# Kernel tuning notes

Measured on AMD Instinct MI355X. Metric: run time of the kernel, lower is better.

The kernel has to match this reference:

```python
import jax, jax.numpy as jnp
import numpy as np

EPS = 1e-5  # torch InstanceNorm2d default eps

def instance_norm(x):
    # per-sample, per-channel normalization over spatial dims (affine=False)
    m = jnp.mean(x, axis=(2, 3), keepdims=True)
    v = jnp.var(x, axis=(2, 3), keepdims=True)
    return (x - m) * jax.lax.rsqrt(v + EPS)

def conv2d(x, w, b, stride, pad):
    y = jax.lax.conv_general_dilated(
        x, w, (stride, stride), [(pad, pad), (pad, pad)],
        dimension_numbers=('NCHW', 'OIHW', 'NCHW'))
    return y + b[None, :, None, None]

def res_block(x, w1, b1, w2, b2):
    out = conv2d(jax.nn.relu(instance_norm(x)), w1, b1, 1, 1)
    out = conv2d(jax.nn.relu(instance_norm(out)), w2, b2, 1, 1)
    return out + x

def res_block_strided(x, w1, b1, w2, b2, ws, bs):
    out = conv2d(jax.nn.relu(instance_norm(x)), w1, b1, 2, 1)
    out = conv2d(jax.nn.relu(instance_norm(out)), w2, b2, 1, 1)
    return out + conv2d(x, ws, bs, 2, 0)  # 1x1 strided skip projection

def setup_inputs() -> dict:
    key = jax.random.key(0)
    ks = jax.random.split(key, 12)
    B, N, C, H, W = 64, 1, 3, 256, 256
    TEXT, EMB, F, HEADS = 256, 512, 32, 5
    FH, FW = H // 16, W // 16  # 16, 16
    def rn(k, shape, scale=0.05):
        return jax.random.normal(k, shape, dtype=jnp.float32) * scale
    z = lambda *s: jnp.zeros(s, jnp.float32)
    return {
        'x': jax.random.normal(ks[0], (B, N, C, H, W), jnp.float32),
        'text_vector': jax.random.normal(ks[1], (B, TEXT), jnp.float32),
        'conv1_w': rn(ks[2], (F, C, 7, 7)),
        'conv1_b': z(F),
        'rbs_w1': rn(ks[3], (3, F, F, 3, 3)),  # 3 strided resblocks
        'rbs_b1': z(3, F),
        'rbs_w2': rn(ks[4], (3, F, F, 3, 3)),
        'rbs_b2': z(3, F),
        'rbs_ws': rn(ks[5], (3, F, F, 1, 1)),
        'rbs_bs': z(3, F),
        'rb_w1': rn(ks[6], (2, F, F, 3, 3)),  # 2 plain resblocks
        'rb_b1': z(2, F),
        'rb_w2': rn(ks[7], (2, F, F, 3, 3)),
        'rb_b2': z(2, F),
        'attn_w': rn(ks[8], (HEADS, FH * FW, TEXT)),  # torch Linear [out,in] per head
        'attn_b': z(HEADS, FH * FW),
        'final_w': rn(ks[9], (EMB, FH * FW * HEADS)),
        'final_b': z(EMB),
    }

def reference(x, text_vector, conv1_w, conv1_b, rbs_w1, rbs_b1, rbs_w2, rbs_b2,
              rbs_ws, rbs_bs, rb_w1, rb_b1, rb_w2, rb_b2, attn_w, attn_b,
              final_w, final_b):
    B, N, C, H, W = x.shape
    feat = x.reshape(B, N * C, H, W)
    feat = instance_norm(feat)
    feat = conv2d(feat, conv1_w, conv1_b, 2, 3)
    # block1 = strided + plain; block2 = strided + plain; block3 = strided
    feat = res_block_strided(feat, rbs_w1[0], rbs_b1[0], rbs_w2[0], rbs_b2[0], rbs_ws[0], rbs_bs[0])
    feat = res_block(feat, rb_w1[0], rb_b1[0], rb_w2[0], rb_b2[0])
    feat = res_block_strided(feat, rbs_w1[1], rbs_b1[1], rbs_w2[1], rbs_b2[1], rbs_ws[1], rbs_bs[1])
    feat = res_block(feat, rb_w1[1], rb_b1[1], rb_w2[1], rb_b2[1])
    feat = res_block_strided(feat, rbs_w1[2], rbs_b1[2], rbs_w2[2], rbs_b2[2], rbs_ws[2], rbs_bs[2])
    # feat: [B, 32, FH, FW]
    HEADS = attn_w.shape[0]
    FH, FW = feat.shape[2], feat.shape[3]
    # sigmoid-gated spatial attention logits per head: [B, HEADS, FH, FW]
    a = jax.nn.sigmoid(jnp.einsum('bt,hot->bho', text_vector, attn_w) + attn_b[None])
    a = a.reshape(B, HEADS, FH, FW)
    # channel scores: spatial sum of gate * feature -> [B, HEADS, C]
    scores = jnp.einsum('bhij,bcij->bhc', a, feat)
    probs = jax.nn.softmax(scores, axis=-1)  # old F.softmax over channel dim
    # weighted channel sum -> per-head attention map [B, HEADS, FH, FW]
    amaps = jnp.einsum('bhc,bcij->bhij', probs, feat)
    out = amaps.reshape(B, -1) @ final_w.T + final_b
    return out
```

## Files before the change

### kernel.cpp

```cpp
#include <hip/hip_runtime.h>
#include <cstdint>
#include <cstddef>

#define INORM_EPS 1e-5f

typedef _Float16 f16;
typedef f16 f16x8 __attribute__((ext_vector_type(8)));
typedef f16 f16x4 __attribute__((ext_vector_type(4)));
typedef float f32x4 __attribute__((ext_vector_type(4)));

__global__ __launch_bounds__(256) void prep(
    const float* __restrict__ rbs_w1, const float* __restrict__ rbs_w2,
    const float* __restrict__ rb_w1, const float* __restrict__ rb_w2,
    const float* __restrict__ rbs_ws, const float* __restrict__ conv1_w,
    float2* __restrict__ SP, f16* __restrict__ wp3, f16* __restrict__ wp1,
    f16* __restrict__ wp7) {
  int i = blockIdx.x * 256 + threadIdx.x;
  if (i < 20672) { SP[i] = make_float2(0.f, 0.f); return; }
  i -= 20672;
  if (i < 92160) {
    int mat = i / 9216, r = i % 9216;
    int p = r >> 10, f = (r >> 9) & 1, l = (r >> 3) & 63, j = r & 7;
    int co = f * 16 + (l & 15), ci = (l >> 4) * 8 + j;
    const float* src; int m;
    if (mat < 3) { src = rbs_w1; m = mat; }
    else if (mat < 6) { src = rbs_w2; m = mat - 3; }
    else if (mat < 8) { src = rb_w1; m = mat - 6; }
    else { src = rb_w2; m = mat - 8; }
    wp3[i] = (f16)src[m * 9216 + co * 288 + ci * 9 + p];
    return;
  }
  i -= 92160;
  if (i < 3072) {
    int mat = i / 1024, r = i % 1024;
    int f = r >> 9, l = (r >> 3) & 63, j = r & 7;
    wp1[i] = (f16)rbs_ws[mat * 1024 + (f * 16 + (l & 15)) * 32 + (l >> 4) * 8 + j];
    return;
  }
  i -= 3072;
  if (i >= 7168) return;
  int ky = i >> 10, f = (i >> 9) & 1, l = (i >> 3) & 63, j = i & 7;
  int k = (l >> 4) * 8 + j, kx = k >> 2, ci = k & 3;
  float v = 0.f;
  if (kx < 7 && ci < 3) v = conv1_w[(f * 16 + (l & 15)) * 147 + ci * 49 + ky * 7 + kx];
  wp7[i] = (f16)v;
}

__global__ __launch_bounds__(256) void stats_raw(const float* __restrict__ in,
                                                 float2* __restrict__ st, int HW) {
  const int map = blockIdx.x >> 3, chunk = blockIdx.x & 7;
  const int n4 = HW >> 5;
  const float4* p = (const float4*)(in + (size_t)map * HW + (size_t)chunk * (HW >> 3));
  float s = 0.f, ss = 0.f;
  for (int i = threadIdx.x; i < n4; i += 256) {
    float4 v = p[i];
    s += v.x + v.y + v.z + v.w;
    ss += v.x * v.x + v.y * v.y + v.z * v.z + v.w * v.w;
  }
  __shared__ float r0[256], r1[256];
  r0[threadIdx.x] = s;
  r1[threadIdx.x] = ss;
  __syncthreads();
  for (int off = 128; off > 0; off >>= 1) {
    if ((int)threadIdx.x < off) {
      r0[threadIdx.x] += r0[threadIdx.x + off];
      r1[threadIdx.x] += r1[threadIdx.x + off];
    }
    __syncthreads();
  }
  if (threadIdx.x == 0) {
    atomicAdd(&st[map].x, r0[0]);
    atomicAdd(&st[map].y, r1[0]);
  }
}

template <int W, int SKIP, int RPB>
__global__ __launch_bounds__(256) void conv3r(
    const f16* __restrict__ Rin, const float2* __restrict__ SPin, float inv_hw,
    const f16* __restrict__ wp, const float* __restrict__ bias,
    const float* __restrict__ bias2, const f16* __restrict__ skip,
    const f16* __restrict__ wps, f16* __restrict__ Rout,
    float2* __restrict__ ostats) {
  constexpr int TPR = W / 16;
  constexpr int LEN = (RPB * TPR) / 4;
  const int t = threadIdx.x, w = t >> 6, l = t & 63;
  const int n = l & 15, q = l >> 4;
  const int b = blockIdx.z;
  const int tx = w % TPR;
  const int y0 = blockIdx.x * RPB + (w / TPR) * LEN;
  const int x = (tx << 4) + n;
  const f16* Rb = Rin + (size_t)b * W * W * 32;

  f16x8 sc, sh;
#pragma unroll
  for (int j = 0; j < 8; j++) {
    float2 s = SPin[b * 32 + q * 8 + j];
    float mean = s.x * inv_hw;
    float rstd = rsqrtf(s.y * inv_hw - mean * mean + INORM_EPS);
    sc[j] = (f16)rstd;
    sh[j] = (f16)(-mean * rstd);
  }

  f16x8 wf[18];
#pragma unroll
  for (int i = 0; i < 18; i++) wf[i] = *(const f16x8*)(wp + i * 512 + l * 8);
  f16x8 wsf0, wsf1;
  if (SKIP == 2) {
    wsf0 = *(const f16x8*)(wps + l * 8);
    wsf1 = *(const f16x8*)(wps + 512 + l * 8);
  }
  float b0 = bias[n], b1 = bias[16 + n];
  if (SKIP == 2) { b0 += bias2[n]; b1 += bias2[16 + n]; }

  f16* ro = Rout + (size_t)b * W * W * 32;
  const f16* sb = skip ? skip + (size_t)b * (SKIP == 2 ? 4 : 1) * W * W * 32 : nullptr;

  bool okc[3];
#pragma unroll
  for (int kx = 0; kx < 3; kx++) okc[kx] = (unsigned)(x + kx - 1) < (unsigned)W;

  auto rowload = [&](int gy, f16x8* dst) {
    int gyc = min(max(gy, 0), W - 1);
#pragma unroll
    for (int kx = 0; kx < 3; kx++) {
      int gxc = min(max(x + kx - 1, 0), W - 1);
      dst[kx] = *(const f16x8*)(Rb + ((size_t)gyc * W + gxc) * 32 + q * 8);
    }
  };
  auto rownorm = [&](int gy, const f16x8* src, f16x8* dst) {
    bool okr = (unsigned)gy < (unsigned)W;
#pragma unroll
    for (int kx = 0; kx < 3; kx++) {
      f16x8 v = src[kx] * sc + sh;
#pragma unroll
      for (int e = 0; e < 8; e++) v[e] = v[e] > (f16)0 ? v[e] : (f16)0;
      f16x8 z = {};
      dst[kx] = (okr && okc[kx]) ? v : z;
    }
  };

  float sm0 = 0.f, sq0 = 0.f, sm1 = 0.f, sq1 = 0.f;
  f16x8 win[9];
  f16x8 pf[2][3];
#pragma unroll
  for (int jj = 0; jj < 3; jj++) rowload(y0 + jj - 1, &win[jj * 3]);
  if (LEN > 1) rowload(y0 + 2, pf[0]);
#pragma unroll
  for (int jj = 0; jj < 3; jj++) rownorm(y0 + jj - 1, &win[jj * 3], &win[jj * 3]);

#pragma unroll
  for (int i = 0; i < LEN; i++) {
    int y = y0 + i;
    if (i + 2 < LEN) rowload(y0 + i + 3, pf[(i + 1) & 1]);
    f32x4 acc0 = {0.f, 0.f, 0.f, 0.f}, acc1 = {0.f, 0.f, 0.f, 0.f};
#pragma unroll
    for (int ky = 0; ky < 3; ky++) {
      int slot = (i + ky) % 3;
#pragma unroll
      for (int kx = 0; kx < 3; kx++) {
        f16x8 a = win[slot * 3 + kx];
        acc0 = __builtin_amdgcn_mfma_f32_16x16x32_f16(a, wf[2 * (ky * 3 + kx)], acc0, 0, 0, 0);
        acc1 = __builtin_amdgcn_mfma_f32_16x16x32_f16(a, wf[2 * (ky * 3 + kx) + 1], acc1, 0, 0, 0);
      }
    }
    if (SKIP == 2) {
      const int Ws = 2 * W;
      f16x8 as = *(const f16x8*)(sb + ((size_t)(2 * y) * Ws + 2 * x) * 32 + q * 8);
      acc0 = __builtin_amdgcn_mfma_f32_16x16x32_f16(as, wsf0, acc0, 0, 0, 0);
      acc1 = __builtin_amdgcn_mfma_f32_16x16x32_f16(as, wsf1, acc1, 0, 0, 0);
    }
#pragma unroll
    for (int r = 0; r < 4; r++) {
      size_t px = (size_t)y * W + (tx << 4) + q * 4 + r;
      float v0 = acc0[r] + b0;
      float v1 = acc1[r] + b1;
      if (SKIP == 1) {
        v0 += (float)sb[px * 32 + n];
        v1 += (float)sb[px * 32 + 16 + n];
      }
      ro[px * 32 + n] = (f16)v0;
      ro[px * 32 + 16 + n] = (f16)v1;
      sm0 += v0; sq0 += v0 * v0;
      sm1 += v1; sq1 += v1 * v1;
    }
    if (i + 1 < LEN) rownorm(y0 + i + 2, pf[i & 1], &win[(i % 3) * 3]);
  }
  if (ostats) {
    sm0 += __shfl_xor(sm0, 16); sm0 += __shfl_xor(sm0, 32);
    sq0 += __shfl_xor(sq0, 16); sq0 += __shfl_xor(sq0, 32);
    sm1 += __shfl_xor(sm1, 16); sm1 += __shfl_xor(sm1, 32);
    sq1 += __shfl_xor(sq1, 16); sq1 += __shfl_xor(sq1, 32);
    if (l < 16) {
      atomicAdd(&ostats[b * 32 + n].x, sm0);
      atomicAdd(&ostats[b * 32 + n].y, sq0);
      atomicAdd(&ostats[b * 32 + 16 + n].x, sm1);
      atomicAdd(&ostats[b * 32 + 16 + n].y, sq1);
    }
  }
}

template <int WIN, int STRIDE, int SKIP, int RPB>
__global__ __launch_bounds__(256) void conv3n(
    const f16* __restrict__ Rin, const float2* __restrict__ SPin, float inv_hw,
    const f16* __restrict__ wp, const float* __restrict__ bias,
    const float* __restrict__ bias2, const f16* __restrict__ skip,
    const f16* __restrict__ wps, f16* __restrict__ Rout,
    float2* __restrict__ ostats) {
  constexpr int WOUT = WIN / STRIDE;
  constexpr int TPR = WOUT / 16;
  constexpr int UNITS = TPR * RPB;
  constexpr int U = UNITS / 4;
  static_assert(U >= 1, "need at least one unit per wave");
  constexpr int NB = (U >= 3) ? 3 : ((U >= 2) ? 2 : 1);
  const int t = threadIdx.x, w = t >> 6, l = t & 63;
  const int n = l & 15, q = l >> 4;
  const int b = blockIdx.z;
  const int yb = blockIdx.x * RPB;
  const f16* Rb = Rin + (size_t)b * WIN * WIN * 32;

  f16x8 sc, sh;
#pragma unroll
  for (int j = 0; j < 8; j++) {
    float2 s = SPin[b * 32 + q * 8 + j];
    float mean = s.x * inv_hw;
    float rstd = rsqrtf(s.y * inv_hw - mean * mean + INORM_EPS);
    sc[j] = (f16)rstd;
    sh[j] = (f16)(-mean * rstd);
  }

  f16x8 wf[18];
#pragma unroll
  for (int i = 0; i < 18; i++) wf[i] = *(const f16x8*)(wp + i * 512 + l * 8);
  f16x8 wsf0, wsf1;
  if (SKIP == 2) {
    wsf0 = *(const f16x8*)(wps + l * 8);
    wsf1 = *(const f16x8*)(wps + 512 + l * 8);
  }
  float b0 = bias[n], b1 = bias[16 + n];
  if (SKIP == 2) { b0 += bias2[n]; b1 += bias2[16 + n]; }

  f16* ro = Rout + (size_t)b * WOUT * WOUT * 32;
  const f16* sb = skip ? skip + (size_t)b * (SKIP == 2 ? 4 : 1) * WOUT * WOUT * 32 : nullptr;

  auto load_u = [&](int u, f16x8* a) {
    int ty = u / TPR, tx = u % TPR;
    int y = yb + ty;
#pragma unroll
    for (int kx = 0; kx < 3; kx++) {
      int gx = STRIDE * ((tx << 4) + n) + kx - 1;
      int gxc = min(max(gx, 0), WIN - 1);
#pragma unroll
      for (int ky = 0; ky < 3; ky++) {
        int gy = STRIDE * y + ky - 1;
        int gyc = min(max(gy, 0), WIN - 1);
        a[ky * 3 + kx] = *(const f16x8*)(Rb + ((size_t)gyc * WIN + gxc) * 32 + q * 8);
      }
    }
  };
  auto norm_u = [&](int u, f16x8* a) {
    int ty = u / TPR, tx = u % TPR;
    int y = yb + ty;
#pragma unroll
    for (int kx = 0; kx < 3; kx++) {
      int gx = STRIDE * ((tx << 4) + n) + kx - 1;
      bool okx = (unsigned)gx < (unsigned)WIN;
#pragma unroll
      for (int ky = 0; ky < 3; ky++) {
        int gy = STRIDE * y + ky - 1;
        bool ok = okx && ((unsigned)gy < (unsigned)WIN);
        f16x8 v = a[ky * 3 + kx] * sc + sh;
#pragma unroll
        for (int e = 0; e < 8; e++) v[e] = v[e] > (f16)0 ? v[e] : (f16)0;
        f16x8 z = {};
        a[ky * 3 + kx] = ok ? v : z;
      }
    }
  };

  float sm0 = 0.f, sq0 = 0.f, sm1 = 0.f, sq1 = 0.f;
  f16x8 buf[NB][9];
  load_u(w, buf[0]);
  if (U > 1) load_u(w + 4, buf[1 % NB]);
#pragma unroll
  for (int i = 0; i < U; i++) {
    int u = w + 4 * i;
    if (i + 2 < U) load_u(u + 8, buf[(i + 2) % NB]);
    f16x8* a = buf[i % NB];
    norm_u(u, a);
    int ty = u / TPR, tx = u % TPR;
    int y = yb + ty, x0 = tx << 4;
    f32x4 acc0 = {0.f, 0.f, 0.f, 0.f}, acc1 = {0.f, 0.f, 0.f, 0.f};
#pragma unroll
    for (int p = 0; p < 9; p++) {
      acc0 = __builtin_amdgcn_mfma_f32_16x16x32_f16(a[p], wf[2 * p], acc0, 0, 0, 0);
      acc1 = __builtin_amdgcn_mfma_f32_16x16x32_f16(a[p], wf[2 * p + 1], acc1, 0, 0, 0);
    }
    if (SKIP == 2) {
      const int Ws = 2 * WOUT;
      f16x8 as = *(const f16x8*)(sb + ((size_t)(2 * y) * Ws + 2 * (x0 + n)) * 32 + q * 8);
      acc0 = __builtin_amdgcn_mfma_f32_16x16x32_f16(as, wsf0, acc0, 0, 0, 0);
      acc1 = __builtin_amdgcn_mfma_f32_16x16x32_f16(as, wsf1, acc1, 0, 0, 0);
    }
#pragma unroll
    for (int r = 0; r < 4; r++) {
      size_t px = (size_t)y * WOUT + x0 + q * 4 + r;
      float v0 = acc0[r] + b0;
      float v1 = acc1[r] + b1;
      if (SKIP == 1) {
        v0 += (float)sb[px * 32 + n];
        v1 += (float)sb[px * 32 + 16 + n];
      }
      ro[px * 32 + n] = (f16)v0;
      ro[px * 32 + 16 + n] = (f16)v1;
      sm0 += v0; sq0 += v0 * v0;
      sm1 += v1; sq1 += v1 * v1;
    }
  }
  if (ostats) {
    sm0 += __shfl_xor(sm0, 16); sm0 += __shfl_xor(sm0, 32);
    sq0 += __shfl_xor(sq0, 16); sq0 += __shfl_xor(sq0, 32);
    sm1 += __shfl_xor(sm1, 16); sm1 += __shfl_xor(sm1, 32);
    sq1 += __shfl_xor(sq1, 16); sq1 += __shfl_xor(sq1, 32);
    if (l < 16) {
      atomicAdd(&ostats[b * 32 + n].x, sm0);
      atomicAdd(&ostats[b * 32 + n].y, sq0);
      atomicAdd(&ostats[b * 32 + 16 + n].x, sm1);
      atomicAdd(&ostats[b * 32 + 16 + n].y, sq1);
    }
  }
}

__global__ __launch_bounds__(256) void conv7(
    const float* __restrict__ x, const float2* __restrict__ SPx,
    const f16* __restrict__ wp, const float* __restrict__ bias,
    f16* __restrict__ Rout, float2* __restrict__ ostats) {
  __shared__ f16 lds[13 * 131 * 8];
  const int t = threadIdx.x, w = t >> 6, l = t & 63;
  const int n = l & 15, q = l >> 4;
  const int b = blockIdx.z;
  const int yb = blockIdx.x * 4;
  const float* Xb = x + (size_t)b * 3 * 65536;
  float mn[3], rs[3];
#pragma unroll
  for (int ci = 0; ci < 3; ci++) {
    float2 s = SPx[b * 3 + ci];
    mn[ci] = s.x * (1.f / 65536.f);
    rs[ci] = rsqrtf(s.y * (1.f / 65536.f) - mn[ci] * mn[ci] + INORM_EPS);
  }
  f16x8 wf[14];
#pragma unroll
  for (int i = 0; i < 14; i++) wf[i] = *(const f16x8*)(wp + i * 512 + l * 8);
  float b0 = bias[n], b1 = bias[16 + n];

  for (int idx = t; idx < 13 * 262; idx += 256) {
    int ri = idx / 262, cl = idx - ri * 262;
    int row = 2 * yb - 3 + ri, col = cl - 3;
    bool ok = ((unsigned)row < 256u) && ((unsigned)col < 256u);
    f16x4 v = {};
    if (ok) {
      const float* p = Xb + (size_t)row * 256 + col;
      v[0] = (f16)((p[0] - mn[0]) * rs[0]);
      v[1] = (f16)((p[65536] - mn[1]) * rs[1]);
      v[2] = (f16)((p[131072] - mn[2]) * rs[2]);
    }
    *(f16x4*)(lds + ((ri * 131 + (cl >> 1)) * 8) + (cl & 1) * 4) = v;
  }
  __syncthreads();

  float sm0 = 0.f, sq0 = 0.f, sm1 = 0.f, sq1 = 0.f;
  f16* ro = Rout + (size_t)b * 16384 * 32;

#pragma unroll
  for (int seg = 0; seg < 2; seg++) {
    const int tx = w + seg * 4;
    const int x0 = tx * 16;
    const int u = x0 + n + q;
#pragma unroll
    for (int i = 0; i < 4; i++) {
      int y = yb + i;
      f32x4 acc0 = {0.f, 0.f, 0.f, 0.f}, acc1 = {0.f, 0.f, 0.f, 0.f};
#pragma unroll
      for (int ky = 0; ky < 7; ky++) {
        f16x8 a = *(const f16x8*)(lds + ((2 * i + ky) * 131 + u) * 8);
        acc0 = __builtin_amdgcn_mfma_f32_16x16x32_f16(a, wf[2 * ky], acc0, 0, 0, 0);
        acc1 = __builtin_amdgcn_mfma_f32_16x16x32_f16(a, wf[2 * ky + 1], acc1, 0, 0, 0);
      }
#pragma unroll
      for (int r = 0; r < 4; r++) {
        size_t px = (size_t)y * 128 + x0 + q * 4 + r;
        float v0 = acc0[r] + b0;
        float v1 = acc1[r] + b1;
        ro[px * 32 + n] = (f16)v0;
        ro[px * 32 + 16 + n] = (f16)v1;
        sm0 += v0; sq0 += v0 * v0;
        sm1 += v1; sq1 += v1 * v1;
      }
    }
  }
  sm0 += __shfl_xor(sm0, 16); sm0 += __shfl_xor(sm0, 32);
  sq0 += __shfl_xor(sq0, 16); sq0 += __shfl_xor(sq0, 32);
  sm1 += __shfl_xor(sm1, 16); sm1 += __shfl_xor(sm1, 32);
  sq1 += __shfl_xor(sq1, 16); sq1 += __shfl_xor(sq1, 32);
  if (l < 16) {
    atomicAdd(&ostats[b * 32 + n].x, sm0);
    atomicAdd(&ostats[b * 32 + n].y, sq0);
    atomicAdd(&ostats[b * 32 + 16 + n].x, sm1);
    atomicAdd(&ostats[b * 32 + 16 + n].y, sq1);
  }
}

__global__ __launch_bounds__(256) void gates_kernel(
    const float* __restrict__ text, const float* __restrict__ attn_w,
    const float* __restrict__ attn_b, float* __restrict__ G) {
  __shared__ float s_text[64 * 257];
  __shared__ float s_w[16 * 256];
  const int t = threadIdx.x, wv = t >> 6, lane = t & 63;
  const int o0 = blockIdx.x * 16;
  for (int d = t; d < 16384; d += 256) {
    int b = d >> 8, k = d & 255;
    s_text[b * 257 + k] = text[d];
  }
  for (int d = t; d < 4096; d += 256) s_w[d] = attn_w[(size_t)o0 * 256 + d];
  __syncthreads();
  float acc[4];
#pragma unroll
  for (int j = 0; j < 4; j++) acc[j] = attn_b[o0 + wv * 4 + j];
  for (int k = 0; k < 256; k++) {
    float tv = s_text[lane * 257 + k];
#pragma unroll
    for (int j = 0; j < 4; j++) acc[j] = fmaf(s_w[(wv * 4 + j) * 256 + k], tv, acc[j]);
  }
#pragma unroll
  for (int j = 0; j < 4; j++) {
    int o = o0 + wv * 4 + j;
    G[o * 64 + lane] = 1.f / (1.f + __expf(-acc[j]));
  }
}

__global__ __launch_bounds__(256) void scores_kernel(
    const f16* __restrict__ feat, const float* __restrict__ G,
    float* __restrict__ amapT) {
  __shared__ float s_feat[256 * 33];
  __shared__ float s_gate[1280];
  __shared__ float s_scores[5 * 32];
  __shared__ float s_probs[5 * 32];
  const int b = blockIdx.x;
  const int t = threadIdx.x;

  for (int i = t; i < 8192; i += 256)
    s_feat[(i >> 5) * 33 + (i & 31)] = (float)feat[(size_t)b * 8192 + i];
  for (int i = t; i < 1280; i += 256) s_gate[i] = G[i * 64 + b];
  __syncthreads();

  if (t < 160) {
    int h = t >> 5, c = t & 31;
    float acc = 0.f;
    for (int ij = 0; ij < 256; ij++) acc += s_gate[h * 256 + ij] * s_feat[ij * 33 + c];
    s_scores[t] = acc;
  }
  __syncthreads();

  if (t < 5) {
    float mx = -1e30f;
    for (int c = 0; c < 32; c++) mx = fmaxf(mx, s_scores[t * 32 + c]);
    float sum = 0.f;
    for (int c = 0; c < 32; c++) {
      float e = __expf(s_scores[t * 32 + c] - mx);
      s_probs[t * 32 + c] = e;
      sum += e;
    }
    float inv = 1.f / sum;
    for (int c = 0; c < 32; c++) s_probs[t * 32 + c] *= inv;
  }
  __syncthreads();

  for (int h = 0; h < 5; h++) {
    float acc = 0.f;
    for (int c = 0; c < 32; c++) acc += s_probs[h * 32 + c] * s_feat[t * 33 + c];
    amapT[(h * 256 + t) * 64 + b] = acc;
  }
}

__global__ __launch_bounds__(256) void final_kernel(
    const float* __restrict__ amapT, const float* __restrict__ final_w,
    const float* __restrict__ final_b, float* __restrict__ out) {
  __shared__ float s_w[4 * 1280];
  __shared__ float s_red[4][4][64];
  const int t = threadIdx.x, wv = t >> 6, lane = t & 63;
  const int e0 = blockIdx.x * 4;
  for (int d = t; d < 5120; d += 256) s_w[d] = final_w[(size_t)e0 * 1280 + d];
  __syncthreads();
  const int k0 = wv * 320;
  float acc[4] = {0.f, 0.f, 0.f, 0.f};
  for (int k = k0; k < k0 + 320; k++) {
    float av = amapT[k * 64 + lane];
#pragma unroll
    for (int e = 0; e < 4; e++) acc[e] = fmaf(s_w[e * 1280 + k], av, acc[e]);
  }
#pragma unroll
  for (int e = 0; e < 4; e++) s_red[wv][e][lane] = acc[e];
  __syncthreads();
  if (wv == 0) {
#pragma unroll
    for (int e = 0; e < 4; e++) {
      float v = s_red[0][e][lane] + s_red[1][e][lane] + s_red[2][e][lane] +
                s_red[3][e][lane] + final_b[e0 + e];
      out[(size_t)lane * 512 + e0 + e] = v;
    }
  }
}

extern "C" void kernel_launch(void* const* d_in, const int* in_sizes, int n_in,
                              void* d_out, int out_size, void* d_ws, size_t ws_size,
                              hipStream_t stream) {
  (void)in_sizes; (void)n_in; (void)out_size; (void)ws_size;
  const float* x       = (const float*)d_in[0];
  const float* text    = (const float*)d_in[1];
  const float* conv1_w = (const float*)d_in[2];
  const float* conv1_b = (const float*)d_in[3];
  const float* rbs_w1  = (const float*)d_in[4];
  const float* rbs_b1  = (const float*)d_in[5];
  const float* rbs_w2  = (const float*)d_in[6];
  const float* rbs_b2  = (const float*)d_in[7];
  const float* rbs_ws  = (const float*)d_in[8];
  const float* rbs_bs  = (const float*)d_in[9];
  const float* rb_w1   = (const float*)d_in[10];
  const float* rb_b1   = (const float*)d_in[11];
  const float* rb_w2   = (const float*)d_in[12];
  const float* rb_b2   = (const float*)d_in[13];
  const float* attn_w  = (const float*)d_in[14];
  const float* attn_b  = (const float*)d_in[15];
  const float* final_w = (const float*)d_in[16];
  const float* final_b = (const float*)d_in[17];
  float* out = (float*)d_out;

  char* wsb = (char*)d_ws;
  f16*   R128 = (f16*)(wsb + 35145728);
  f16*   R64a = (f16*)(wsb + 102254592);
  f16*   R64b = (f16*)(wsb + 119031808);
  f16*   R64c = (f16*)(wsb + 135809024);
  f16*   R32a = (f16*)(wsb + 152586240);
  f16*   R32b = (f16*)(wsb + 156780544);
  f16*   R32c = (f16*)(wsb + 160974848);
  f16*   R16a = (f16*)(wsb + 165169152);
  f16*   R16b = (f16*)(wsb + 166217728);
  float2* SP  = (float2*)(wsb + 167266304);
  float2* SPx = (float2*)(wsb + 167430144);
  f16*   wp3  = (f16*)(wsb + 167431680);
  f16*   wp1  = (f16*)(wsb + 167616000);
  f16*   wp7  = (f16*)(wsb + 167622144);
  float* G     = (float*)(wsb + 167636480);
  float* amapT = (float*)(wsb + 167964160);
  float2* SP0 = SP + 0 * 2048;
  float2* SP1 = SP + 1 * 2048;
  float2* SP2 = SP + 2 * 2048;
  float2* SP3 = SP + 3 * 2048;
  float2* SP4 = SP + 4 * 2048;
  float2* SP5 = SP + 5 * 2048;
  float2* SP6 = SP + 6 * 2048;
  float2* SP7 = SP + 7 * 2048;
  float2* SP8 = SP + 8 * 2048;
  float2* SP9 = SP + 9 * 2048;

  prep<<<481, 256, 0, stream>>>(rbs_w1, rbs_w2, rb_w1, rb_w2, rbs_ws, conv1_w,
                                SP, wp3, wp1, wp7);
  stats_raw<<<1536, 256, 0, stream>>>(x, SPx, 65536);

  conv7<<<dim3(32, 1, 64), 256, 0, stream>>>(x, SPx, wp7, conv1_b, R128, SP0);

  conv3n<128, 2, 0, 4><<<dim3(16, 1, 64), 256, 0, stream>>>(
      R128, SP0, 1.f / 16384.f, wp3, rbs_b1, nullptr, nullptr, nullptr, R64a, SP1);
  conv3r<64, 2, 4><<<dim3(16, 1, 64), 256, 0, stream>>>(
      R64a, SP1, 1.f / 4096.f, wp3 + 3 * 9216, rbs_b2, rbs_bs, R128, wp1, R64b, SP2);

  conv3r<64, 0, 4><<<dim3(16, 1, 64), 256, 0, stream>>>(
      R64b, SP2, 1.f / 4096.f, wp3 + 6 * 9216, rb_b1, nullptr, nullptr, nullptr, R64c, SP3);
  conv3r<64, 1, 4><<<dim3(16, 1, 64), 256, 0, stream>>>(
      R64c, SP3, 1.f / 4096.f, wp3 + 8 * 9216, rb_b2, nullptr, R64b, nullptr, R64a, SP4);

  conv3n<64, 2, 0, 4><<<dim3(8, 1, 64), 256, 0, stream>>>(
      R64a, SP4, 1.f / 4096.f, wp3 + 1 * 9216, rbs_b1 + 32, nullptr, nullptr, nullptr, R32a, SP5);
  conv3r<32, 2, 2><<<dim3(16, 1, 64), 256, 0, stream>>>(
      R32a, SP5, 1.f / 1024.f, wp3 + 4 * 9216, rbs_b2 + 32, rbs_bs + 32, R64a, wp1 + 1024, R32b, SP6);

  conv3r<32, 0, 2><<<dim3(16, 1, 64), 256, 0, stream>>>(
      R32b, SP6, 1.f / 1024.f, wp3 + 7 * 9216, rb_b1 + 32, nullptr, nullptr, nullptr, R32c, SP7);
  conv3r<32, 1, 2><<<dim3(16, 1, 64), 256, 0, stream>>>(
      R32c, SP7, 1.f / 1024.f, wp3 + 9 * 9216, rb_b2 + 32, nullptr, R32b, nullptr, R32a, SP8);

  conv3n<32, 2, 0, 4><<<dim3(4, 1, 64), 256, 0, stream>>>(
      R32a, SP8, 1.f / 1024.f, wp3 + 2 * 9216, rbs_b1 + 64, nullptr, nullptr, nullptr, R16a, SP9);
  conv3n<16, 1, 2, 4><<<dim3(4, 1, 64), 256, 0, stream>>>(
      R16a, SP9, 1.f / 256.f, wp3 + 5 * 9216, rbs_b2 + 64, rbs_bs + 64, R32a, wp1 + 2048, R16b, nullptr);

  gates_kernel<<<80, 256, 0, stream>>>(text, attn_w, attn_b, G);
  scores_kernel<<<64, 256, 0, stream>>>(R16b, G, amapT);
  final_kernel<<<128, 256, 0, stream>>>(amapT, final_w, final_b, out);
}
```

Baseline: 362.5 us.

## Add LDS-staged stride-2 conv kernel and split conv7 across column halves

Adds a new conv3s2l kernel for the stride-2 3x3 convolutions. It stages the normalized and ReLU'd input tile in LDS with even and odd columns de-interleaved, so each MFMA operand is a contiguous LDS read, and it applies the normalize/ReLU once per element. This replaces conv3n for the first two strided blocks, using two x-halves for the 128 input. conv7 is also split across two column halves, which doubles the grid and shrinks the per-block LDS footprint to raise occupancy, at the cost of re-reading halo columns.

```diff
diff --git a/kernel.cpp b/kernel.cpp
--- a/kernel.cpp
+++ b/kernel.cpp
@@ -330,15 +330,110 @@
   }
 }
 
+template <int WIN>
+__global__ __launch_bounds__(256) void conv3s2l(
+    const f16* __restrict__ Rin, const float2* __restrict__ SPin, float inv_hw,
+    const f16* __restrict__ wp, const float* __restrict__ bias,
+    f16* __restrict__ Rout, float2* __restrict__ ostats) {
+  constexpr int WOUT = WIN / 2;
+  __shared__ f16 lds[4 * 9 * 66 * 8];
+  const int t = threadIdx.x, w = t >> 6, l = t & 63;
+  const int n = l & 15, q = l >> 4;
+  const int b = blockIdx.z;
+  const int yb = blockIdx.x * 4;
+  const int xh = blockIdx.y;
+  const f16* Rb = Rin + (size_t)b * WIN * WIN * 32;
+
+  const int qs = t & 3;
+  f16x8 scs, shs;
+#pragma unroll
+  for (int j = 0; j < 8; j++) {
+    float2 s = SPin[b * 32 + qs * 8 + j];
+    float mean = s.x * inv_hw;
+    float rstd = rsqrtf(s.y * inv_hw - mean * mean + INORM_EPS);
+    scs[j] = (f16)rstd;
+    shs[j] = (f16)(-mean * rstd);
+  }
+
+  for (int idx = t; idx < 2340; idx += 256) {
+    int ri = idx / 260, rem = idx - ri * 260;
+    int lc = rem >> 2;
+    int gr = 2 * yb - 1 + ri, gc = 64 * xh - 1 + lc;
+    bool ok = ((unsigned)gr < (unsigned)WIN) && ((unsigned)gc < (unsigned)WIN);
+    int grc = ok ? gr : 0, gcc = ok ? gc : 0;
+    f16x8 v = *(const f16x8*)(Rb + ((size_t)grc * WIN + gcc) * 32 + qs * 8);
+    v = v * scs + shs;
+#pragma unroll
+    for (int e = 0; e < 8; e++) v[e] = v[e] > (f16)0 ? v[e] : (f16)0;
+    f16x8 z = {};
+    if (!ok) v = z;
+    int sl = (lc & 1) ? (lc >> 1) : 32 + (lc >> 1);
+    *(f16x8*)(lds + qs * 4752 + (ri * 66 + sl) * 8) = v;
+  }
+
+  f16x8 wf[18];
+#pragma unroll
+  for (int i = 0; i < 18; i++) wf[i] = *(const f16x8*)(wp + i * 512 + l * 8);
+  float b0 = bias[n], b1 = bias[16 + n];
+  __syncthreads();
+
+  float sm0 = 0.f, sq0 = 0.f, sm1 = 0.f, sq1 = 0.f;
+  f16* ro = Rout + (size_t)b * WOUT * WOUT * 32;
+  const f16* lq = lds + q * 4752;
+
+#pragma unroll
+  for (int i = 0; i < 2; i++) {
+    int u = w + 4 * i;
+    int ty = u >> 1, tx = u & 1;
+    int m = tx * 16 + n;
+    f32x4 acc0 = {0.f, 0.f, 0.f, 0.f}, acc1 = {0.f, 0.f, 0.f, 0.f};
+#pragma unroll
+    for (int ky = 0; ky < 3; ky++) {
+      int ri = 2 * ty + ky;
+      f16x8 a0 = *(const f16x8*)(lq + (ri * 66 + 32 + m) * 8);
+      f16x8 a1 = *(const f16x8*)(lq + (ri * 66 + m) * 8);
+      f16x8 a2 = *(const f16x8*)(lq + (ri * 66 + 33 + m) * 8);
+      acc0 = __builtin_amdgcn_mfma_f32_16x16x32_f16(a0, wf[2 * (ky * 3 + 0)], acc0, 0, 0, 0);
+      acc1 = __builtin_amdgcn_mfma_f32_16x16x32_f16(a0, wf[2 * (ky * 3 + 0) + 1], acc1, 0, 0, 0);
+      acc0 = __builtin_amdgcn_mfma_f32_16x16x32_f16(a1, wf[2 * (ky * 3 + 1)], acc0, 0, 0, 0);
+      acc1 = __builtin_amdgcn_mfma_f32_16x16x32_f16(a1, wf[2 * (ky * 3 + 1) + 1], acc1, 0, 0, 0);
+      acc0 = __builtin_amdgcn_mfma_f32_16x16x32_f16(a2, wf[2 * (ky * 3 + 2)], acc0, 0, 0, 0);
+      acc1 = __builtin_amdgcn_mfma_f32_16x16x32_f16(a2, wf[2 * (ky * 3 + 2) + 1], acc1, 0, 0, 0);
+    }
+    int y = yb + ty, x0 = xh * 32 + tx * 16;
+#pragma unroll
+    for (int r = 0; r < 4; r++) {
+      size_t px = (size_t)y * WOUT + x0 + q * 4 + r;
+      float v0 = acc0[r] + b0;
+      float v1 = acc1[r] + b1;
+      ro[px * 32 + n] = (f16)v0;
+      ro[px * 32 + 16 + n] = (f16)v1;
+      sm0 += v0; sq0 += v0 * v0;
+      sm1 += v1; sq1 += v1 * v1;
+    }
+  }
+  sm0 += __shfl_xor(sm0, 16); sm0 += __shfl_xor(sm0, 32);
+  sq0 += __shfl_xor(sq0, 16); sq0 += __shfl_xor(sq0, 32);
+  sm1 += __shfl_xor(sm1, 16); sm1 += __shfl_xor(sm1, 32);
+  sq1 += __shfl_xor(sq1, 16); sq1 += __shfl_xor(sq1, 32);
+  if (l < 16) {
+    atomicAdd(&ostats[b * 32 + n].x, sm0);
+    atomicAdd(&ostats[b * 32 + n].y, sq0);
+    atomicAdd(&ostats[b * 32 + 16 + n].x, sm1);
+    atomicAdd(&ostats[b * 32 + 16 + n].y, sq1);
+  }
+}
+
 __global__ __launch_bounds__(256) void conv7(
     const float* __restrict__ x, const float2* __restrict__ SPx,
     const f16* __restrict__ wp, const float* __restrict__ bias,
     f16* __restrict__ Rout, float2* __restrict__ ostats) {
-  __shared__ f16 lds[13 * 131 * 8];
+  __shared__ f16 lds[13 * 67 * 8];
   const int t = threadIdx.x, w = t >> 6, l = t & 63;
   const int n = l & 15, q = l >> 4;
   const int b = blockIdx.z;
   const int yb = blockIdx.x * 4;
+  const int xh = blockIdx.y;
   const float* Xb = x + (size_t)b * 3 * 65536;
   float mn[3], rs[3];
 #pragma unroll
@@ -352,9 +447,9 @@
   for (int i = 0; i < 14; i++) wf[i] = *(const f16x8*)(wp + i * 512 + l * 8);
   float b0 = bias[n], b1 = bias[16 + n];
 
-  for (int idx = t; idx < 13 * 262; idx += 256) {
-    int ri = idx / 262, cl = idx - ri * 262;
-    int row = 2 * yb - 3 + ri, col = cl - 3;
+  for (int idx = t; idx < 13 * 134; idx += 256) {
+    int ri = idx / 134, cl = idx - ri * 134;
+    int row = 2 * yb - 3 + ri, col = 128 * xh - 3 + cl;
     bool ok = ((unsigned)row < 256u) && ((unsigned)col < 256u);
     f16x4 v = {};
     if (ok) {
@@ -363,38 +458,34 @@
       v[1] = (f16)((p[65536] - mn[1]) * rs[1]);
       v[2] = (f16)((p[131072] - mn[2]) * rs[2]);
     }
-    *(f16x4*)(lds + ((ri * 131 + (cl >> 1)) * 8) + (cl & 1) * 4) = v;
+    *(f16x4*)(lds + ((ri * 67 + (cl >> 1)) * 8) + (cl & 1) * 4) = v;
   }
   __syncthreads();
 
   float sm0 = 0.f, sq0 = 0.f, sm1 = 0.f, sq1 = 0.f;
   f16* ro = Rout + (size_t)b * 16384 * 32;
 
-#pragma unroll
-  for (int seg = 0; seg < 2; seg++) {
-    const int tx = w + seg * 4;
-    const int x0 = tx * 16;
-    const int u = x0 + n + q;
-#pragma unroll
-    for (int i = 0; i < 4; i++) {
-      int y = yb + i;
-      f32x4 acc0 = {0.f, 0.f, 0.f, 0.f}, acc1 = {0.f, 0.f, 0.f, 0.f};
-#pragma unroll
-      for (int ky = 0; ky < 7; ky++) {
-        f16x8 a = *(const f16x8*)(lds + ((2 * i + ky) * 131 + u) * 8);
-        acc0 = __builtin_amdgcn_mfma_f32_16x16x32_f16(a, wf[2 * ky], acc0, 0, 0, 0);
-        acc1 = __builtin_amdgcn_mfma_f32_16x16x32_f16(a, wf[2 * ky + 1], acc1, 0, 0, 0);
-      }
-#pragma unroll
-      for (int r = 0; r < 4; r++) {
-        size_t px = (size_t)y * 128 + x0 + q * 4 + r;
-        float v0 = acc0[r] + b0;
-        float v1 = acc1[r] + b1;
-        ro[px * 32 + n] = (f16)v0;
-        ro[px * 32 + 16 + n] = (f16)v1;
-        sm0 += v0; sq0 += v0 * v0;
-        sm1 += v1; sq1 += v1 * v1;
-      }
+  const int x0 = xh * 64 + w * 16;
+  const int u = w * 16 + n + q;
+#pragma unroll
+  for (int i = 0; i < 4; i++) {
+    int y = yb + i;
+    f32x4 acc0 = {0.f, 0.f, 0.f, 0.f}, acc1 = {0.f, 0.f, 0.f, 0.f};
+#pragma unroll
+    for (int ky = 0; ky < 7; ky++) {
+      f16x8 a = *(const f16x8*)(lds + ((2 * i + ky) * 67 + u) * 8);
+      acc0 = __builtin_amdgcn_mfma_f32_16x16x32_f16(a, wf[2 * ky], acc0, 0, 0, 0);
+      acc1 = __builtin_amdgcn_mfma_f32_16x16x32_f16(a, wf[2 * ky + 1], acc1, 0, 0, 0);
+    }
+#pragma unroll
+    for (int r = 0; r < 4; r++) {
+      size_t px = (size_t)y * 128 + x0 + q * 4 + r;
+      float v0 = acc0[r] + b0;
+      float v1 = acc1[r] + b1;
+      ro[px * 32 + n] = (f16)v0;
+      ro[px * 32 + 16 + n] = (f16)v1;
+      sm0 += v0; sq0 += v0 * v0;
+      sm1 += v1; sq1 += v1 * v1;
     }
   }
   sm0 += __shfl_xor(sm0, 16); sm0 += __shfl_xor(sm0, 32);
@@ -566,10 +657,10 @@
                                 SP, wp3, wp1, wp7);
   stats_raw<<<1536, 256, 0, stream>>>(x, SPx, 65536);
 
-  conv7<<<dim3(32, 1, 64), 256, 0, stream>>>(x, SPx, wp7, conv1_b, R128, SP0);
-
-  conv3n<128, 2, 0, 4><<<dim3(16, 1, 64), 256, 0, stream>>>(
-      R128, SP0, 1.f / 16384.f, wp3, rbs_b1, nullptr, nullptr, nullptr, R64a, SP1);
+  conv7<<<dim3(32, 2, 64), 256, 0, stream>>>(x, SPx, wp7, conv1_b, R128, SP0);
+
+  conv3s2l<128><<<dim3(16, 2, 64), 256, 0, stream>>>(
+      R128, SP0, 1.f / 16384.f, wp3, rbs_b1, R64a, SP1);
   conv3r<64, 2, 4><<<dim3(16, 1, 64), 256, 0, stream>>>(
       R64a, SP1, 1.f / 4096.f, wp3 + 3 * 9216, rbs_b2, rbs_bs, R128, wp1, R64b, SP2);
 
@@ -578,8 +669,8 @@
   conv3r<64, 1, 4><<<dim3(16, 1, 64), 256, 0, stream>>>(
       R64c, SP3, 1.f / 4096.f, wp3 + 8 * 9216, rb_b2, nullptr, R64b, nullptr, R64a, SP4);
 
-  conv3n<64, 2, 0, 4><<<dim3(8, 1, 64), 256, 0, stream>>>(
-      R64a, SP4, 1.f / 4096.f, wp3 + 1 * 9216, rbs_b1 + 32, nullptr, nullptr, nullptr, R32a, SP5);
+  conv3s2l<64><<<dim3(8, 1, 64), 256, 0, stream>>>(
+      R64a, SP4, 1.f / 4096.f, wp3 + 1 * 9216, rbs_b1 + 32, R32a, SP5);
   conv3r<32, 2, 2><<<dim3(16, 1, 64), 256, 0, stream>>>(
       R32a, SP5, 1.f / 1024.f, wp3 + 4 * 9216, rbs_b2 + 32, rbs_bs + 32, R64a, wp1 + 1024, R32b, SP6);
 
```

After: 391.2 us. +7.9%, slower.

## Merge input stats into prep kernel and double rows per conv block

Applied to the files above, without the earlier changes.

Folds the raw-input statistics reduction into the weight-prep kernel as extra blocks. Each block now writes a per-chunk partial sum instead of using atomics, and conv7 reduces the 8 partials itself, which removes a launch and the dependency on zeroed SPx. The conv3r/conv3n launches also double rows-per-block, halving grid size, to cut redundant halo and weight loads per block. The risks are lower occupancy and parallelism at small spatial sizes (e.g. only 2x64 blocks for the 16/32 stages) and a larger workspace region at offset 0.

```diff
diff --git a/kernel.cpp b/kernel.cpp
--- a/kernel.cpp
+++ b/kernel.cpp
@@ -9,15 +9,41 @@
 typedef f16 f16x4 __attribute__((ext_vector_type(4)));
 typedef float f32x4 __attribute__((ext_vector_type(4)));
 
-__global__ __launch_bounds__(256) void prep(
+__global__ __launch_bounds__(256) void prep_stats(
     const float* __restrict__ rbs_w1, const float* __restrict__ rbs_w2,
     const float* __restrict__ rb_w1, const float* __restrict__ rb_w2,
     const float* __restrict__ rbs_ws, const float* __restrict__ conv1_w,
-    float2* __restrict__ SP, f16* __restrict__ wp3, f16* __restrict__ wp1,
-    f16* __restrict__ wp7) {
-  int i = blockIdx.x * 256 + threadIdx.x;
-  if (i < 20672) { SP[i] = make_float2(0.f, 0.f); return; }
-  i -= 20672;
+    const float* __restrict__ x, float2* __restrict__ SP,
+    f16* __restrict__ wp3, f16* __restrict__ wp1, f16* __restrict__ wp7,
+    float2* __restrict__ SPx8) {
+  const int bx = blockIdx.x;
+  if (bx >= 480) {
+    const int g = bx - 480;
+    const int map = g >> 3, chunk = g & 7;
+    const float4* p = (const float4*)(x + (size_t)map * 65536 + (size_t)chunk * 8192);
+    float s = 0.f, ss = 0.f;
+    for (int i = threadIdx.x; i < 2048; i += 256) {
+      float4 v = p[i];
+      s += v.x + v.y + v.z + v.w;
+      ss += v.x * v.x + v.y * v.y + v.z * v.z + v.w * v.w;
+    }
+    __shared__ float r0[256], r1[256];
+    r0[threadIdx.x] = s;
+    r1[threadIdx.x] = ss;
+    __syncthreads();
+    for (int off = 128; off > 0; off >>= 1) {
+      if ((int)threadIdx.x < off) {
+        r0[threadIdx.x] += r0[threadIdx.x + off];
+        r1[threadIdx.x] += r1[threadIdx.x + off];
+      }
+      __syncthreads();
+    }
+    if (threadIdx.x == 0) SPx8[map * 8 + chunk] = make_float2(r0[0], r1[0]);
+    return;
+  }
+  int i = bx * 256 + threadIdx.x;
+  if (i < 20480) { SP[i] = make_float2(0.f, 0.f); return; }
+  i -= 20480;
   if (i < 92160) {
     int mat = i / 9216, r = i % 9216;
     int p = r >> 10, f = (r >> 9) & 1, l = (r >> 3) & 63, j = r & 7;
@@ -44,34 +70,6 @@
   float v = 0.f;
   if (kx < 7 && ci < 3) v = conv1_w[(f * 16 + (l & 15)) * 147 + ci * 49 + ky * 7 + kx];
   wp7[i] = (f16)v;
-}
-
-__global__ __launch_bounds__(256) void stats_raw(const float* __restrict__ in,
-                                                 float2* __restrict__ st, int HW) {
-  const int map = blockIdx.x >> 3, chunk = blockIdx.x & 7;
-  const int n4 = HW >> 5;
-  const float4* p = (const float4*)(in + (size_t)map * HW + (size_t)chunk * (HW >> 3));
-  float s = 0.f, ss = 0.f;
-  for (int i = threadIdx.x; i < n4; i += 256) {
-    float4 v = p[i];
-    s += v.x + v.y + v.z + v.w;
-    ss += v.x * v.x + v.y * v.y + v.z * v.z + v.w * v.w;
-  }
-  __shared__ float r0[256], r1[256];
-  r0[threadIdx.x] = s;
-  r1[threadIdx.x] = ss;
-  __syncthreads();
-  for (int off = 128; off > 0; off >>= 1) {
-    if ((int)threadIdx.x < off) {
-      r0[threadIdx.x] += r0[threadIdx.x + off];
-      r1[threadIdx.x] += r1[threadIdx.x + off];
-    }
-    __syncthreads();
-  }
-  if (threadIdx.x == 0) {
-    atomicAdd(&st[map].x, r0[0]);
-    atomicAdd(&st[map].y, r1[0]);
-  }
 }
 
 template <int W, int SKIP, int RPB>
@@ -331,7 +329,7 @@
 }
 
 __global__ __launch_bounds__(256) void conv7(
-    const float* __restrict__ x, const float2* __restrict__ SPx,
+    const float* __restrict__ x, const float2* __restrict__ SPx8,
     const f16* __restrict__ wp, const float* __restrict__ bias,
     f16* __restrict__ Rout, float2* __restrict__ ostats) {
   __shared__ f16 lds[13 * 131 * 8];
@@ -343,9 +341,14 @@
   float mn[3], rs[3];
 #pragma unroll
   for (int ci = 0; ci < 3; ci++) {
-    float2 s = SPx[b * 3 + ci];
-    mn[ci] = s.x * (1.f / 65536.f);
-    rs[ci] = rsqrtf(s.y * (1.f / 65536.f) - mn[ci] * mn[ci] + INORM_EPS);
+    float sx = 0.f, sxx = 0.f;
+#pragma unroll
+    for (int c = 0; c < 8; c++) {
+      float2 v = SPx8[(b * 3 + ci) * 8 + c];
+      sx += v.x; sxx += v.y;
+    }
+    mn[ci] = sx * (1.f / 65536.f);
+    rs[ci] = rsqrtf(sxx * (1.f / 65536.f) - mn[ci] * mn[ci] + INORM_EPS);
   }
   f16x8 wf[14];
 #pragma unroll
@@ -535,6 +538,7 @@
   float* out = (float*)d_out;
 
   char* wsb = (char*)d_ws;
+  float2* SPx8 = (float2*)(wsb + 0);
   f16*   R128 = (f16*)(wsb + 35145728);
   f16*   R64a = (f16*)(wsb + 102254592);
   f16*   R64b = (f16*)(wsb + 119031808);
@@ -545,7 +549,6 @@
   f16*   R16a = (f16*)(wsb + 165169152);
   f16*   R16b = (f16*)(wsb + 166217728);
   float2* SP  = (float2*)(wsb + 167266304);
-  float2* SPx = (float2*)(wsb + 167430144);
   f16*   wp3  = (f16*)(wsb + 167431680);
   f16*   wp1  = (f16*)(wsb + 167616000);
   f16*   wp7  = (f16*)(wsb + 167622144);
@@ -562,35 +565,34 @@
   float2* SP8 = SP + 8 * 2048;
   float2* SP9 = SP + 9 * 2048;
 
-  prep<<<481, 256, 0, stream>>>(rbs_w1, rbs_w2, rb_w1, rb_w2, rbs_ws, conv1_w,
-                                SP, wp3, wp1, wp7);
-  stats_raw<<<1536, 256, 0, stream>>>(x, SPx, 65536);
-
-  conv7<<<dim3(32, 1, 64), 256, 0, stream>>>(x, SPx, wp7, conv1_b, R128, SP0);
+  prep_stats<<<2016, 256, 0, stream>>>(rbs_w1, rbs_w2, rb_w1, rb_w2, rbs_ws,
+                                       conv1_w, x, SP, wp3, wp1, wp7, SPx8);
+
+  conv7<<<dim3(32, 1, 64), 256, 0, stream>>>(x, SPx8, wp7, conv1_b, R128, SP0);
 
   conv3n<128, 2, 0, 4><<<dim3(16, 1, 64), 256, 0, stream>>>(
       R128, SP0, 1.f / 16384.f, wp3, rbs_b1, nullptr, nullptr, nullptr, R64a, SP1);
-  conv3r<64, 2, 4><<<dim3(16, 1, 64), 256, 0, stream>>>(
+  conv3r<64, 2, 8><<<dim3(8, 1, 64), 256, 0, stream>>>(
       R64a, SP1, 1.f / 4096.f, wp3 + 3 * 9216, rbs_b2, rbs_bs, R128, wp1, R64b, SP2);
 
-  conv3r<64, 0, 4><<<dim3(16, 1, 64), 256, 0, stream>>>(
+  conv3r<64, 0, 8><<<dim3(8, 1, 64), 256, 0, stream>>>(
       R64b, SP2, 1.f / 4096.f, wp3 + 6 * 9216, rb_b1, nullptr, nullptr, nullptr, R64c, SP3);
-  conv3r<64, 1, 4><<<dim3(16, 1, 64), 256, 0, stream>>>(
+  conv3r<64, 1, 8><<<dim3(8, 1, 64), 256, 0, stream>>>(
       R64c, SP3, 1.f / 4096.f, wp3 + 8 * 9216, rb_b2, nullptr, R64b, nullptr, R64a, SP4);
 
   conv3n<64, 2, 0, 4><<<dim3(8, 1, 64), 256, 0, stream>>>(
       R64a, SP4, 1.f / 4096.f, wp3 + 1 * 9216, rbs_b1 + 32, nullptr, nullptr, nullptr, R32a, SP5);
-  conv3r<32, 2, 2><<<dim3(16, 1, 64), 256, 0, stream>>>(
+  conv3r<32, 2, 8><<<dim3(4, 1, 64), 256, 0, stream>>>(
       R32a, SP5, 1.f / 1024.f, wp3 + 4 * 9216, rbs_b2 + 32, rbs_bs + 32, R64a, wp1 + 1024, R32b, SP6);
 
-  conv3r<32, 0, 2><<<dim3(16, 1, 64), 256, 0, stream>>>(
+  conv3r<32, 0, 8><<<dim3(4, 1, 64), 256, 0, stream>>>(
       R32b, SP6, 1.f / 1024.f, wp3 + 7 * 9216, rb_b1 + 32, nullptr, nullptr, nullptr, R32c, SP7);
-  conv3r<32, 1, 2><<<dim3(16, 1, 64), 256, 0, stream>>>(
+  conv3r<32, 1, 8><<<dim3(4, 1, 64), 256, 0, stream>>>(
       R32c, SP7, 1.f / 1024.f, wp3 + 9 * 9216, rb_b2 + 32, nullptr, R32b, nullptr, R32a, SP8);
 
-  conv3n<32, 2, 0, 4><<<dim3(4, 1, 64), 256, 0, stream>>>(
+  conv3n<32, 2, 0, 8><<<dim3(2, 1, 64), 256, 0, stream>>>(
       R32a, SP8, 1.f / 1024.f, wp3 + 2 * 9216, rbs_b1 + 64, nullptr, nullptr, nullptr, R16a, SP9);
-  conv3n<16, 1, 2, 4><<<dim3(4, 1, 64), 256, 0, stream>>>(
+  conv3n<16, 1, 2, 8><<<dim3(2, 1, 64), 256, 0, stream>>>(
       R16a, SP9, 1.f / 256.f, wp3 + 5 * 9216, rbs_b2 + 64, rbs_bs + 64, R32a, wp1 + 2048, R16b, nullptr);
 
   gates_kernel<<<80, 256, 0, stream>>>(text, attn_w, attn_b, G);
```

New measurement: 320.8 us. 11.5% less time.
